# Performance work log

Hardware: AMD Instinct MI355X
Metric: run time of the kernel (lower is better)

## Reference

```python
import jax, jax.numpy as jnp
import numpy as np

B, T, D, H = 2, 2048, 1024, 16
HD = D // H  # head_dim = 64

def setup_inputs() -> dict:
    key = jax.random.key(0)
    ks = jax.random.split(key, 5)
    s = 0.02
    return {
        "x": jax.random.normal(ks[0], (B, T, D), dtype=jnp.float32),
        "w_qkv": jax.random.normal(ks[1], (3 * D, D), dtype=jnp.float32) * s,
        "b_qkv": jax.random.normal(ks[2], (3 * D,), dtype=jnp.float32) * s,
        "w_proj": jax.random.normal(ks[3], (D, D), dtype=jnp.float32) * s,
        "b_proj": jax.random.normal(ks[4], (D,), dtype=jnp.float32) * s,
    }

def reference(x, w_qkv, b_qkv, w_proj, b_proj):
    b, t, c = x.shape
    h, hd = H, HD
    scale = hd ** -0.5
    # qkv projection (torch Linear: x @ W^T + b)
    qkv = x @ w_qkv.T + b_qkv                      # [b, t, 3c]
    q, k, v = jnp.split(qkv, 3, axis=-1)
    # b t (h d) -> b h t d
    reshape = lambda z: z.reshape(b, t, h, hd).transpose(0, 2, 1, 3)
    q, k, v = reshape(q), reshape(k), reshape(v)
    scores = jnp.einsum("bhqd,bhkd->bhqk", q, k) * scale  # [b, h, t, t]
    causal = jnp.triu(jnp.ones((t, t), dtype=bool), k=1)   # True above diag
    scores = jnp.where(causal[None, None], -jnp.inf, scores)
    attn = jax.nn.softmax(scores, axis=-1)
    out = jnp.einsum("bhqk,bhkd->bhqd", attn, v)            # [b, h, t, d]
    out = out.transpose(0, 2, 1, 3).reshape(b, t, c)        # b h t d -> b t (h d)
    return out @ w_proj.T + b_proj
```

## Files before the change

kernel.cpp:

```cpp
#include <hip/hip_runtime.h>
#include <hip/hip_bf16.h>

#define Bq 2
#define Tq 2048
#define Dq 1024
#define Hq 16
#define HDq 64

typedef __attribute__((ext_vector_type(8))) short short8;
typedef __attribute__((ext_vector_type(4))) float f32x4;

__device__ __forceinline__ unsigned short f2bf(float f) {
  union { float f; unsigned int i; } v; v.f = f;
  unsigned int r = v.i + 0x7fffu + ((v.i >> 16) & 1u);
  return (unsigned short)(r >> 16);
}

__device__ __forceinline__ short8 cvt8(const float* __restrict__ g) {
  const float4* gp = (const float4*)g;
  float4 x0 = gp[0], x1 = gp[1];
  short8 v;
  v[0] = (short)f2bf(x0.x); v[1] = (short)f2bf(x0.y);
  v[2] = (short)f2bf(x0.z); v[3] = (short)f2bf(x0.w);
  v[4] = (short)f2bf(x1.x); v[5] = (short)f2bf(x1.y);
  v[6] = (short)f2bf(x1.z); v[7] = (short)f2bf(x1.w);
  return v;
}

__device__ __forceinline__ void async_cp16(const void* g, void* l) {
  __builtin_amdgcn_global_load_lds(
      (const __attribute__((address_space(1))) void*)g,
      (__attribute__((address_space(3))) void*)l, 16, 0, 0);
}

__device__ __forceinline__ void permswap(unsigned &a, unsigned &b) {
  asm("v_permlane32_swap_b32 %0, %1" : "+v"(a), "+v"(b));
  asm("v_permlane16_swap_b32 %0, %1" : "+v"(a), "+v"(b));
}

constexpr int NXC = (Bq * Tq * Dq) / 8;
constexpr int NW1C = (3 * Dq * Dq) / 8;
constexpr int NW2C = (Dq * Dq) / 8;

#define QSCL 0.18033688011112042f

__global__ __launch_bounds__(256)
void cvt_all(const float* __restrict__ x, const float* __restrict__ w1,
             const float* __restrict__ w2, unsigned short* __restrict__ xo,
             unsigned short* __restrict__ w1o, unsigned short* __restrict__ w2o)
{
  int i = blockIdx.x * 256 + threadIdx.x;
  const float* src; unsigned short* dst; int j;
  if (i < NXC)              { src = x;  dst = xo;  j = i; }
  else if (i < NXC + NW1C)  { src = w1; dst = w1o; j = i - NXC; }
  else                      { src = w2; dst = w2o; j = i - NXC - NW1C; }
  *(short8*)&dst[(size_t)j * 8] = cvt8(src + (size_t)j * 8);
}

template<int EPI, int BM_, int BN_>
__global__ __launch_bounds__(256)
void gemm_bt(const unsigned short* __restrict__ Ab, const unsigned short* __restrict__ Wb,
             const float* __restrict__ bias, float* __restrict__ outp,
             int K, int N,
             unsigned short* __restrict__ qo, unsigned short* __restrict__ ko,
             unsigned short* __restrict__ vo)
{
  constexpr int WM = BM_ / 2, WN = BN_ / 2;
  constexpr int NI = WM / 16;
  constexpr int NJ = WN / 16;
  constexpr int NAI = BM_ / 32;
  constexpr int NBI = BN_ / 32;
  __shared__ unsigned short As[2 * BM_ * 32];
  __shared__ unsigned short Bs[2 * BN_ * 32];

  const int t = threadIdx.x;
  const int lane = t & 63, w = t >> 6;
  const int m0 = blockIdx.y * BM_, n0 = blockIdx.x * BN_;
  const int fr = lane & 15, qd = lane >> 4;
  const int wm = (w >> 1) * WM, wn = (w & 1) * WN;

  f32x4 acc[NI][NJ] = {};

  for (int k0 = 0; k0 < K; k0 += 64) {
    __syncthreads();
    #pragma unroll
    for (int j = 0; j < NAI; j++) {
      int G = j * 256 + t;
      int panel = G / (BM_ * 4), rowg = (G / 4) % BM_, colg = G & 3;
      async_cp16(Ab + (size_t)(m0 + rowg) * K + k0 + panel * 32 + colg * 8, &As[G * 8]);
    }
    #pragma unroll
    for (int j = 0; j < NBI; j++) {
      int G = j * 256 + t;
      int panel = G / (BN_ * 4), rowg = (G / 4) % BN_, colg = G & 3;
      async_cp16(Wb + (size_t)(n0 + rowg) * K + k0 + panel * 32 + colg * 8, &Bs[G * 8]);
    }
    __syncthreads();
    #pragma unroll
    for (int kh = 0; kh < 2; kh++) {
      short8 af[NI], bf[NJ];
      #pragma unroll
      for (int ib = 0; ib < NI; ib++)
        af[ib] = *(const short8*)&As[kh * (BM_ * 32) + (wm + ib * 16 + fr) * 32 + qd * 8];
      #pragma unroll
      for (int jb = 0; jb < NJ; jb++)
        bf[jb] = *(const short8*)&Bs[kh * (BN_ * 32) + (wn + jb * 16 + fr) * 32 + qd * 8];
      #pragma unroll
      for (int ib = 0; ib < NI; ib++)
        #pragma unroll
        for (int jb = 0; jb < NJ; jb++)
          acc[ib][jb] = __builtin_amdgcn_mfma_f32_16x16x32_bf16(af[ib], bf[jb], acc[ib][jb], 0, 0, 0);
    }
  }

  #pragma unroll
  for (int jb = 0; jb < NJ; jb++) {
    int col = n0 + wn + jb * 16 + fr;
    float bv = bias[col];
    if (EPI == 0) {
      int which = col >> 10;
      int rem = col & 1023;
      int hh = rem >> 6, dd = rem & 63;
      #pragma unroll
      for (int ib = 0; ib < NI; ib++) {
        int row4 = m0 + wm + ib * 16 + qd * 4;
        int bb = row4 >> 11, tt = row4 & (Tq - 1);
        if (which == 2) {
          unsigned lo = (unsigned)f2bf(acc[ib][jb][0] + bv)
                      | ((unsigned)f2bf(acc[ib][jb][1] + bv) << 16);
          unsigned hi = (unsigned)f2bf(acc[ib][jb][2] + bv)
                      | ((unsigned)f2bf(acc[ib][jb][3] + bv) << 16);
          uint2 pk; pk.x = lo; pk.y = hi;
          *(uint2*)&vo[((size_t)(bb * Hq + hh) * HDq + dd) * Tq + tt] = pk;
        } else {
          unsigned short* dst = (which == 0) ? qo : ko;
          float scl = (which == 0) ? QSCL : 1.0f;
          #pragma unroll
          for (int r = 0; r < 4; r++)
            dst[((size_t)(bb * Hq + hh) * Tq + tt + r) * HDq + dd] =
                f2bf((acc[ib][jb][r] + bv) * scl);
        }
      }
    } else {
      #pragma unroll
      for (int ib = 0; ib < NI; ib++)
        #pragma unroll
        for (int r = 0; r < 4; r++) {
          int row = m0 + wm + ib * 16 + qd * 4 + r;
          outp[(size_t)row * N + col] = acc[ib][jb][r] + bv;
        }
    }
  }
}


template<bool DIAG>
__device__ __forceinline__ void strip_iter(
    const unsigned short* __restrict__ Ksb, const unsigned short* __restrict__ Vtsb,
    const short8 (&aq)[2], const short8 ones,
    int fr, int qd, int off0, int off1, int thr,
    f32x4 (&oacc)[4], f32x4& lacc)
{
  short8 bk[4][2];
  #pragma unroll
  for (int nb = 0; nb < 4; nb++) {
    bk[nb][0] = *(const short8*)&Ksb[(nb * 16 + fr) * 64 + off0];
    bk[nb][1] = *(const short8*)&Ksb[(nb * 16 + fr) * 64 + off1];
  }
  f32x4 s4[4] = {};
  __builtin_amdgcn_s_setprio(1);
  #pragma unroll
  for (int nb = 0; nb < 4; nb++)
    s4[nb] = __builtin_amdgcn_mfma_f32_16x16x32_bf16(bk[nb][0], aq[0], s4[nb], 0, 0, 0);
  #pragma unroll
  for (int nb = 0; nb < 4; nb++)
    s4[nb] = __builtin_amdgcn_mfma_f32_16x16x32_bf16(bk[nb][1], aq[1], s4[nb], 0, 0, 0);
  __builtin_amdgcn_s_setprio(0);

  unsigned x[4][2];
  #pragma unroll
  for (int nb = 0; nb < 4; nb++) {
    float p[4];
    #pragma unroll
    for (int reg = 0; reg < 4; reg++) {
      p[reg] = exp2f(s4[nb][reg]);
      if (DIAG && (nb * 16 + qd * 4 + reg) > thr) p[reg] = 0.f;
    }
    asm("v_cvt_pk_bf16_f32 %0, %1, %2" : "=v"(x[nb][0]) : "v"(p[0]), "v"(p[1]));
    asm("v_cvt_pk_bf16_f32 %0, %1, %2" : "=v"(x[nb][1]) : "v"(p[2]), "v"(p[3]));
  }
  permswap(x[0][0], x[1][0]);
  permswap(x[0][1], x[1][1]);
  permswap(x[2][0], x[3][0]);
  permswap(x[2][1], x[3][1]);

  short8 ap0, ap1;
  {
    union { unsigned u[4]; short8 s; } c0, c1;
    c0.u[0] = x[0][0]; c0.u[1] = x[0][1]; c0.u[2] = x[1][0]; c0.u[3] = x[1][1];
    c1.u[0] = x[2][0]; c1.u[1] = x[2][1]; c1.u[2] = x[3][0]; c1.u[3] = x[3][1];
    ap0 = c0.s; ap1 = c1.s;
  }

  short8 bv[4][2];
  #pragma unroll
  for (int db = 0; db < 4; db++) {
    bv[db][0] = *(const short8*)&Vtsb[(db * 16 + fr) * 64 + off0];
    bv[db][1] = *(const short8*)&Vtsb[(db * 16 + fr) * 64 + off1];
  }
  __builtin_amdgcn_s_setprio(1);
  lacc = __builtin_amdgcn_mfma_f32_16x16x32_bf16(ap0, ones, lacc, 0, 0, 0);
  lacc = __builtin_amdgcn_mfma_f32_16x16x32_bf16(ap1, ones, lacc, 0, 0, 0);
  #pragma unroll
  for (int db = 0; db < 4; db++) {
    oacc[db] = __builtin_amdgcn_mfma_f32_16x16x32_bf16(ap0, bv[db][0], oacc[db], 0, 0, 0);
    oacc[db] = __builtin_amdgcn_mfma_f32_16x16x32_bf16(ap1, bv[db][1], oacc[db], 0, 0, 0);
  }
  __builtin_amdgcn_s_setprio(0);
}

__global__ __launch_bounds__(256, 4)
void attn_fwd(const unsigned short* __restrict__ qb, const unsigned short* __restrict__ kb,
              const unsigned short* __restrict__ vtb, unsigned short* __restrict__ ab)
{
  __shared__ unsigned short Ks[2][64 * 64];
  __shared__ unsigned short Vts[2][64 * 64];

  const int t = threadIdx.x, w = t >> 6, lane = t & 63;
  const int fr = lane & 15, qd = lane >> 4;
  const int bh = blockIdx.x;
  const int s = 31 - (int)blockIdx.y;
  const int s0 = s * 64;
  const int thr = w * 16 + fr;

  short8 aq[2];
  const unsigned short* Qg = qb + ((size_t)bh * Tq + s0) * HDq;
  #pragma unroll
  for (int c = 0; c < 2; c++)
    aq[c] = *(const short8*)(Qg + (w * 16 + fr) * 64 + c * 32 + qd * 8);

  const unsigned short* Kbh = kb + (size_t)bh * Tq * HDq;
  const unsigned short* Vbh = vtb + (size_t)bh * HDq * Tq;

  const int off0 = ((qd ^ (fr & 7)) * 8);
  const int off1 = off0 ^ 32;

  const int G0 = 2 * w * 64 + lane, G1 = G0 + 64;
  const int r0 = G0 >> 3, g0 = (G0 & 7) ^ (r0 & 7);
  const int r1 = G1 >> 3, g1 = (G1 & 7) ^ (r1 & 7);

  short8 ones;
  #pragma unroll
  for (int j = 0; j < 8; j++) ones[j] = (short)0x3F80;

  f32x4 oacc[4] = {};
  f32x4 lacc = {};

  async_cp16(Kbh + (size_t)r0 * 64 + g0 * 8, &Ks[0][G0 * 8]);
  async_cp16(Vbh + (size_t)r0 * Tq + g0 * 8, &Vts[0][G0 * 8]);
  async_cp16(Kbh + (size_t)r1 * 64 + g1 * 8, &Ks[0][G1 * 8]);
  async_cp16(Vbh + (size_t)r1 * Tq + g1 * 8, &Vts[0][G1 * 8]);

  for (int kt = 0; kt < s; kt++) {
    const int cur = kt & 1, nxt = cur ^ 1;
    __syncthreads();
    const size_t kofs = (size_t)(kt + 1) * 64;
    async_cp16(Kbh + (kofs + r0) * 64 + g0 * 8, &Ks[nxt][G0 * 8]);
    async_cp16(Vbh + (size_t)r0 * Tq + kofs + g0 * 8, &Vts[nxt][G0 * 8]);
    async_cp16(Kbh + (kofs + r1) * 64 + g1 * 8, &Ks[nxt][G1 * 8]);
    async_cp16(Vbh + (size_t)r1 * Tq + kofs + g1 * 8, &Vts[nxt][G1 * 8]);
    strip_iter<false>(Ks[cur], Vts[cur], aq, ones, fr, qd, off0, off1, thr, oacc, lacc);
  }
  __syncthreads();
  strip_iter<true>(Ks[s & 1], Vts[s & 1], aq, ones, fr, qd, off0, off1, thr, oacc, lacc);

  #pragma unroll
  for (int reg = 0; reg < 4; reg++) {
    float linv = 1.0f / lacc[reg];
    size_t rowoff = ((size_t)(bh >> 4) * Tq + s0 + w * 16 + qd * 4 + reg) * Dq
                  + (bh & 15) * HDq;
    #pragma unroll
    for (int db = 0; db < 4; db++)
      ab[rowoff + db * 16 + fr] = f2bf(oacc[db][reg] * linv);
  }
}

extern "C" void kernel_launch(void* const* d_in, const int* in_sizes, int n_in,
                              void* d_out, int out_size, void* d_ws, size_t ws_size,
                              hipStream_t stream) {
  const float* x      = (const float*)d_in[0];
  const float* w_qkv  = (const float*)d_in[1];
  const float* b_qkv  = (const float*)d_in[2];
  const float* w_proj = (const float*)d_in[3];
  const float* b_proj = (const float*)d_in[4];
  float* out = (float*)d_out;

  unsigned short* ws = (unsigned short*)d_ws;
  const size_t NE = (size_t)Bq * Hq * Tq * HDq;
  unsigned short* qb  = ws;
  unsigned short* kb  = ws + NE;
  unsigned short* vtb = ws + 2 * NE;
  unsigned short* ab  = ws + 3 * NE;
  unsigned short* xb  = ws + 4 * NE;
  unsigned short* wqb = xb + (size_t)NXC * 8;
  unsigned short* wpb = wqb + (size_t)NW1C * 8;

  dim3 blk(256);
  cvt_all<<<dim3((NXC + NW1C + NW2C) >> 8), blk, 0, stream>>>(x, w_qkv, w_proj, xb, wqb, wpb);

  dim3 g1(3 * Dq / 128, Bq * Tq / 128);
  gemm_bt<0, 128, 128><<<g1, blk, 0, stream>>>(xb, wqb, b_qkv, nullptr,
                                               Dq, 3 * Dq, qb, kb, vtb);
  dim3 g2(Bq * Hq, Tq / 64);
  attn_fwd<<<g2, blk, 0, stream>>>(qb, kb, vtb, ab);
  dim3 g3(Dq / 128, Bq * Tq / 64);
  gemm_bt<1, 64, 128><<<g3, blk, 0, stream>>>(ab, wpb, b_proj, out,
                                              Dq, Dq, nullptr, nullptr, nullptr);
}
```

Baseline: 175.0 us.

## Add 256x256 eight-wave QKV GEMM with phased async staging and MFMA priority

Replaces the 128x128 QKV projection GEMM with a dedicated 256x256-tile kernel using 512 threads (8 waves), a 64-wide K step, XOR-swizzled LDS, and a double buffer whose next-tile loads are split into four phases interleaved with MFMA blocks under raised scheduling priority. The aim is more data reuse per tile and better overlap of global loads with matrix math in the largest GEMM. The trade-off is only 12x16=192 blocks (fewer than CUs per wave of launch on MI355X), heavy register and LDS use (128 KB shared), and many barriers per K step.

```diff
diff --git a/kernel.cpp b/kernel.cpp
--- a/kernel.cpp
+++ b/kernel.cpp
@@ -55,6 +55,145 @@
   else if (i < NXC + NW1C)  { src = w1; dst = w1o; j = i - NXC; }
   else                      { src = w2; dst = w2o; j = i - NXC - NW1C; }
   *(short8*)&dst[(size_t)j * 8] = cvt8(src + (size_t)j * 8);
+}
+
+
+__global__ __launch_bounds__(512, 2)
+void gemm_qkv_8p(const unsigned short* __restrict__ Ab,
+                 const unsigned short* __restrict__ Wb,
+                 const float* __restrict__ bias, int K,
+                 unsigned short* __restrict__ qo, unsigned short* __restrict__ ko,
+                 unsigned short* __restrict__ vo)
+{
+  __shared__ unsigned short As[2][256 * 64];
+  __shared__ unsigned short Bs[2][256 * 64];
+
+  const int t = threadIdx.x;
+  const int lane = t & 63, w = t >> 6;
+  const int fr = lane & 15, qd = lane >> 4;
+  const int wmi = w >> 2, wni = w & 3;
+  const int m0 = blockIdx.y * 256, n0 = blockIdx.x * 256;
+  const int arow_base = wmi * 128;
+  const int brow_base = wni * 64;
+
+  const int Gr0 = t >> 3;
+  const int Gr1 = 64 + Gr0;
+  const int Gc  = (t & 7) ^ (Gr0 & 7);
+
+#define STAGE_HALF(kt1, hh, bufi) do {                                         \
+    const unsigned short* _sb = ((hh) < 2) ? Ab + (size_t)m0 * K               \
+                                           : Wb + (size_t)n0 * K;              \
+    unsigned short* _lb = ((hh) < 2) ? &As[bufi][0] : &Bs[bufi][0];            \
+    const int _h = (hh) & 1;                                                   \
+    async_cp16(_sb + (size_t)(_h * 128 + Gr0) * K + (kt1) * 64 + Gc * 8,       \
+               _lb + _h * 8192 + t * 8);                                       \
+    async_cp16(_sb + (size_t)(_h * 128 + Gr1) * K + (kt1) * 64 + Gc * 8,       \
+               _lb + _h * 8192 + 4096 + t * 8);                                \
+  } while (0)
+
+#define READ_AF(rg) do {                                                       \
+    _Pragma("unroll")                                                          \
+    for (int ibs = 0; ibs < 4; ibs++) {                                        \
+      const int r = arow_base + (rg) * 64 + ibs * 16 + fr;                     \
+      af[ibs][0] = *(const short8*)&As[c][r * 64 + ((qd ^ (r & 7)) * 8)];      \
+      af[ibs][1] = *(const short8*)&As[c][r * 64 + (((4 + qd) ^ (r & 7)) * 8)];\
+    } } while (0)
+
+#define READ_BF(cg) do {                                                       \
+    _Pragma("unroll")                                                          \
+    for (int jbs = 0; jbs < 2; jbs++) {                                        \
+      const int r = brow_base + (cg) * 32 + jbs * 16 + fr;                     \
+      bf[jbs][0] = *(const short8*)&Bs[c][r * 64 + ((qd ^ (r & 7)) * 8)];      \
+      bf[jbs][1] = *(const short8*)&Bs[c][r * 64 + (((4 + qd) ^ (r & 7)) * 8)];\
+    } } while (0)
+
+#define MM16(rg, cg) do {                                                      \
+    __builtin_amdgcn_s_setprio(1);                                             \
+    _Pragma("unroll")                                                          \
+    for (int ibs = 0; ibs < 4; ibs++)                                          \
+      _Pragma("unroll")                                                        \
+      for (int jbs = 0; jbs < 2; jbs++) {                                      \
+        acc[(rg)*4+ibs][(cg)*2+jbs] = __builtin_amdgcn_mfma_f32_16x16x32_bf16( \
+            af[ibs][0], bf[jbs][0], acc[(rg)*4+ibs][(cg)*2+jbs], 0, 0, 0);     \
+        acc[(rg)*4+ibs][(cg)*2+jbs] = __builtin_amdgcn_mfma_f32_16x16x32_bf16( \
+            af[ibs][1], bf[jbs][1], acc[(rg)*4+ibs][(cg)*2+jbs], 0, 0, 0);     \
+      }                                                                        \
+    __builtin_amdgcn_s_setprio(0); } while (0)
+
+#define BAR() do { asm volatile("" ::: "memory");                              \
+    __builtin_amdgcn_s_barrier(); asm volatile("" ::: "memory"); } while (0)
+
+  f32x4 acc[8][4] = {};
+  short8 af[4][2], bf[2][2];
+
+  STAGE_HALF(0, 0, 0); STAGE_HALF(0, 1, 0);
+  STAGE_HALF(0, 2, 0); STAGE_HALF(0, 3, 0);
+
+  const int KT = K >> 6;
+  for (int kt = 0; kt < KT; kt++) {
+    const int c = kt & 1;
+    const bool pf = (kt + 1 < KT);
+    if (pf) {
+      STAGE_HALF(kt + 1, 0, c ^ 1);
+      asm volatile("s_waitcnt vmcnt(2)" ::: "memory");
+    } else {
+      asm volatile("s_waitcnt vmcnt(0)" ::: "memory");
+    }
+    __builtin_amdgcn_s_barrier();
+    READ_AF(0); READ_BF(0);
+    BAR();
+    MM16(0, 0);
+    BAR();
+    READ_BF(1);
+    if (pf) STAGE_HALF(kt + 1, 1, c ^ 1);
+    BAR();
+    MM16(0, 1);
+    BAR();
+    READ_AF(1);
+    if (pf) STAGE_HALF(kt + 1, 2, c ^ 1);
+    BAR();
+    MM16(1, 1);
+    BAR();
+    READ_BF(0);
+    if (pf) STAGE_HALF(kt + 1, 3, c ^ 1);
+    BAR();
+    MM16(1, 0);
+    BAR();
+  }
+
+  #pragma unroll
+  for (int jb = 0; jb < 4; jb++) {
+    int col = n0 + wni * 64 + jb * 16 + fr;
+    float bv = bias[col];
+    int which = col >> 10;
+    int rem = col & 1023;
+    int hh = rem >> 6, dd = rem & 63;
+    #pragma unroll
+    for (int ib = 0; ib < 8; ib++) {
+      int row4 = m0 + wmi * 128 + ib * 16 + qd * 4;
+      int bb = row4 >> 11, tt = row4 & (Tq - 1);
+      if (which == 2) {
+        unsigned lo = (unsigned)f2bf(acc[ib][jb][0] + bv)
+                    | ((unsigned)f2bf(acc[ib][jb][1] + bv) << 16);
+        unsigned hi = (unsigned)f2bf(acc[ib][jb][2] + bv)
+                    | ((unsigned)f2bf(acc[ib][jb][3] + bv) << 16);
+        uint2 pk; pk.x = lo; pk.y = hi;
+        *(uint2*)&vo[((size_t)(bb * Hq + hh) * HDq + dd) * Tq + tt] = pk;
+      } else {
+        unsigned short* dst = (which == 0) ? qo : ko;
+        float scl = (which == 0) ? QSCL : 1.0f;
+        #pragma unroll
+        for (int r = 0; r < 4; r++)
+          dst[((size_t)(bb * Hq + hh) * Tq + tt + r) * HDq + dd] =
+              f2bf((acc[ib][jb][r] + bv) * scl);
+      }
+    }
+  }
+#undef STAGE_HALF
+#undef READ_AF
+#undef READ_BF
+#undef MM16
+#undef BAR
 }
 
 template<int EPI, int BM_, int BN_>
@@ -308,11 +447,12 @@
   dim3 blk(256);
   cvt_all<<<dim3((NXC + NW1C + NW2C) >> 8), blk, 0, stream>>>(x, w_qkv, w_proj, xb, wqb, wpb);
 
-  dim3 g1(3 * Dq / 128, Bq * Tq / 128);
-  gemm_bt<0, 128, 128><<<g1, blk, 0, stream>>>(xb, wqb, b_qkv, nullptr,
-                                               Dq, 3 * Dq, qb, kb, vtb);
+  dim3 g1(3 * Dq / 256, Bq * Tq / 256);
+  gemm_qkv_8p<<<g1, dim3(512), 0, stream>>>(xb, wqb, b_qkv, Dq, qb, kb, vtb);
+
   dim3 g2(Bq * Hq, Tq / 64);
   attn_fwd<<<g2, blk, 0, stream>>>(qb, kb, vtb, ab);
+
   dim3 g3(Dq / 128, Bq * Tq / 64);
   gemm_bt<1, 64, 128><<<g3, blk, 0, stream>>>(ab, wpb, b_proj, out,
                                               Dq, Dq, nullptr, nullptr, nullptr);
```

After: 180.5 us. 1.03x slower.

## Pair short and long causal query strips per block to balance attention work

Applied to the files above, without the earlier changes.

Each attention block now handles two query strips, p and 31-p. They share the same K/V tiles loaded into shared memory, so every block gets equal work under the causal mask and K/V reuse doubles for the overlapping prefix. The grid halves to 16 x 32 blocks and launch bounds drop to 2 blocks per CU to make room for the doubled accumulators and Q fragments. The cost is higher register pressure, lower occupancy and fewer blocks in flight.

```diff
diff --git a/kernel.cpp b/kernel.cpp
--- a/kernel.cpp
+++ b/kernel.cpp
@@ -155,7 +155,7 @@
 
 
 template<bool DIAG>
-__device__ __forceinline__ void strip_iter(
+__device__ __forceinline__ void strip_one(
     const unsigned short* __restrict__ Ksb, const unsigned short* __restrict__ Vtsb,
     const short8 (&aq)[2], const short8 ones,
     int fr, int qd, int off0, int off1, int thr,
@@ -219,7 +219,88 @@
   __builtin_amdgcn_s_setprio(0);
 }
 
-__global__ __launch_bounds__(256, 4)
+template<bool SMALLDIAG>
+__device__ __forceinline__ void strip_dual(
+    const unsigned short* __restrict__ Ksb, const unsigned short* __restrict__ Vtsb,
+    const short8 (&aqB)[2], const short8 (&aqA)[2], const short8 ones,
+    int fr, int qd, int off0, int off1, int thr,
+    f32x4 (&oB)[4], f32x4& lB, f32x4 (&oA)[4], f32x4& lA)
+{
+  short8 bk[4][2];
+  #pragma unroll
+  for (int nb = 0; nb < 4; nb++) {
+    bk[nb][0] = *(const short8*)&Ksb[(nb * 16 + fr) * 64 + off0];
+    bk[nb][1] = *(const short8*)&Ksb[(nb * 16 + fr) * 64 + off1];
+  }
+  f32x4 sB[4] = {}, sA[4] = {};
+  __builtin_amdgcn_s_setprio(1);
+  #pragma unroll
+  for (int nb = 0; nb < 4; nb++) {
+    sB[nb] = __builtin_amdgcn_mfma_f32_16x16x32_bf16(bk[nb][0], aqB[0], sB[nb], 0, 0, 0);
+    sA[nb] = __builtin_amdgcn_mfma_f32_16x16x32_bf16(bk[nb][0], aqA[0], sA[nb], 0, 0, 0);
+  }
+  #pragma unroll
+  for (int nb = 0; nb < 4; nb++) {
+    sB[nb] = __builtin_amdgcn_mfma_f32_16x16x32_bf16(bk[nb][1], aqB[1], sB[nb], 0, 0, 0);
+    sA[nb] = __builtin_amdgcn_mfma_f32_16x16x32_bf16(bk[nb][1], aqA[1], sA[nb], 0, 0, 0);
+  }
+  __builtin_amdgcn_s_setprio(0);
+
+  unsigned xB[4][2], xA[4][2];
+  #pragma unroll
+  for (int nb = 0; nb < 4; nb++) {
+    float pB[4], pA[4];
+    #pragma unroll
+    for (int reg = 0; reg < 4; reg++) {
+      pB[reg] = exp2f(sB[nb][reg]);
+      pA[reg] = exp2f(sA[nb][reg]);
+      if (SMALLDIAG && (nb * 16 + qd * 4 + reg) > thr) pA[reg] = 0.f;
+    }
+    asm("v_cvt_pk_bf16_f32 %0, %1, %2" : "=v"(xB[nb][0]) : "v"(pB[0]), "v"(pB[1]));
+    asm("v_cvt_pk_bf16_f32 %0, %1, %2" : "=v"(xB[nb][1]) : "v"(pB[2]), "v"(pB[3]));
+    asm("v_cvt_pk_bf16_f32 %0, %1, %2" : "=v"(xA[nb][0]) : "v"(pA[0]), "v"(pA[1]));
+    asm("v_cvt_pk_bf16_f32 %0, %1, %2" : "=v"(xA[nb][1]) : "v"(pA[2]), "v"(pA[3]));
+  }
+  permswap(xB[0][0], xB[1][0]); permswap(xB[0][1], xB[1][1]);
+  permswap(xB[2][0], xB[3][0]); permswap(xB[2][1], xB[3][1]);
+  permswap(xA[0][0], xA[1][0]); permswap(xA[0][1], xA[1][1]);
+  permswap(xA[2][0], xA[3][0]); permswap(xA[2][1], xA[3][1]);
+
+  short8 apB0, apB1, apA0, apA1;
+  {
+    union { unsigned u[4]; short8 s; } c0, c1, c2, c3;
+    c0.u[0] = xB[0][0]; c0.u[1] = xB[0][1]; c0.u[2] = xB[1][0]; c0.u[3] = xB[1][1];
+    c1.u[0] = xB[2][0]; c1.u[1] = xB[2][1]; c1.u[2] = xB[3][0]; c1.u[3] = xB[3][1];
+    c2.u[0] = xA[0][0]; c2.u[1] = xA[0][1]; c2.u[2] = xA[1][0]; c2.u[3] = xA[1][1];
+    c3.u[0] = xA[2][0]; c3.u[1] = xA[2][1]; c3.u[2] = xA[3][0]; c3.u[3] = xA[3][1];
+    apB0 = c0.s; apB1 = c1.s; apA0 = c2.s; apA1 = c3.s;
+  }
+
+  short8 bv[4][2];
+  #pragma unroll
+  for (int db = 0; db < 4; db++) {
+    bv[db][0] = *(const short8*)&Vtsb[(db * 16 + fr) * 64 + off0];
+    bv[db][1] = *(const short8*)&Vtsb[(db * 16 + fr) * 64 + off1];
+  }
+  __builtin_amdgcn_s_setprio(1);
+  lB = __builtin_amdgcn_mfma_f32_16x16x32_bf16(apB0, ones, lB, 0, 0, 0);
+  lA = __builtin_amdgcn_mfma_f32_16x16x32_bf16(apA0, ones, lA, 0, 0, 0);
+  lB = __builtin_amdgcn_mfma_f32_16x16x32_bf16(apB1, ones, lB, 0, 0, 0);
+  lA = __builtin_amdgcn_mfma_f32_16x16x32_bf16(apA1, ones, lA, 0, 0, 0);
+  #pragma unroll
+  for (int db = 0; db < 4; db++) {
+    oB[db] = __builtin_amdgcn_mfma_f32_16x16x32_bf16(apB0, bv[db][0], oB[db], 0, 0, 0);
+    oA[db] = __builtin_amdgcn_mfma_f32_16x16x32_bf16(apA0, bv[db][0], oA[db], 0, 0, 0);
+  }
+  #pragma unroll
+  for (int db = 0; db < 4; db++) {
+    oB[db] = __builtin_amdgcn_mfma_f32_16x16x32_bf16(apB1, bv[db][1], oB[db], 0, 0, 0);
+    oA[db] = __builtin_amdgcn_mfma_f32_16x16x32_bf16(apA1, bv[db][1], oA[db], 0, 0, 0);
+  }
+  __builtin_amdgcn_s_setprio(0);
+}
+
+__global__ __launch_bounds__(256, 2)
 void attn_fwd(const unsigned short* __restrict__ qb, const unsigned short* __restrict__ kb,
               const unsigned short* __restrict__ vtb, unsigned short* __restrict__ ab)
 {
@@ -228,16 +309,22 @@
 
   const int t = threadIdx.x, w = t >> 6, lane = t & 63;
   const int fr = lane & 15, qd = lane >> 4;
-  const int bh = blockIdx.x;
-  const int s = 31 - (int)blockIdx.y;
-  const int s0 = s * 64;
+  const int p = blockIdx.x;
+  const int bh = blockIdx.y;
+  const int sB = 31 - p, sA = p;
+  const int s0t[2] = { sB * 64, sA * 64 };
   const int thr = w * 16 + fr;
 
-  short8 aq[2];
-  const unsigned short* Qg = qb + ((size_t)bh * Tq + s0) * HDq;
-  #pragma unroll
-  for (int c = 0; c < 2; c++)
-    aq[c] = *(const short8*)(Qg + (w * 16 + fr) * 64 + c * 32 + qd * 8);
+  short8 aqB[2], aqA[2];
+  {
+    const unsigned short* QgB = qb + ((size_t)bh * Tq + s0t[0]) * HDq;
+    const unsigned short* QgA = qb + ((size_t)bh * Tq + s0t[1]) * HDq;
+    #pragma unroll
+    for (int c = 0; c < 2; c++) {
+      aqB[c] = *(const short8*)(QgB + (w * 16 + fr) * 64 + c * 32 + qd * 8);
+      aqA[c] = *(const short8*)(QgA + (w * 16 + fr) * 64 + c * 32 + qd * 8);
+    }
+  }
 
   const unsigned short* Kbh = kb + (size_t)bh * Tq * HDq;
   const unsigned short* Vbh = vtb + (size_t)bh * HDq * Tq;
@@ -253,35 +340,53 @@
   #pragma unroll
   for (int j = 0; j < 8; j++) ones[j] = (short)0x3F80;
 
-  f32x4 oacc[4] = {};
-  f32x4 lacc = {};
+  f32x4 oB[4] = {}, oA[4] = {};
+  f32x4 lB = {}, lA = {};
 
   async_cp16(Kbh + (size_t)r0 * 64 + g0 * 8, &Ks[0][G0 * 8]);
   async_cp16(Vbh + (size_t)r0 * Tq + g0 * 8, &Vts[0][G0 * 8]);
   async_cp16(Kbh + (size_t)r1 * 64 + g1 * 8, &Ks[0][G1 * 8]);
   async_cp16(Vbh + (size_t)r1 * Tq + g1 * 8, &Vts[0][G1 * 8]);
 
-  for (int kt = 0; kt < s; kt++) {
-    const int cur = kt & 1, nxt = cur ^ 1;
+  for (int kt = 0; kt <= sB; kt++) {
+    const int cur = kt & 1;
     __syncthreads();
-    const size_t kofs = (size_t)(kt + 1) * 64;
-    async_cp16(Kbh + (kofs + r0) * 64 + g0 * 8, &Ks[nxt][G0 * 8]);
-    async_cp16(Vbh + (size_t)r0 * Tq + kofs + g0 * 8, &Vts[nxt][G0 * 8]);
-    async_cp16(Kbh + (kofs + r1) * 64 + g1 * 8, &Ks[nxt][G1 * 8]);
-    async_cp16(Vbh + (size_t)r1 * Tq + kofs + g1 * 8, &Vts[nxt][G1 * 8]);
-    strip_iter<false>(Ks[cur], Vts[cur], aq, ones, fr, qd, off0, off1, thr, oacc, lacc);
-  }
-  __syncthreads();
-  strip_iter<true>(Ks[s & 1], Vts[s & 1], aq, ones, fr, qd, off0, off1, thr, oacc, lacc);
+    if (kt < sB) {
+      const int nxt = cur ^ 1;
+      const size_t kofs = (size_t)(kt + 1) * 64;
+      async_cp16(Kbh + (kofs + r0) * 64 + g0 * 8, &Ks[nxt][G0 * 8]);
+      async_cp16(Vbh + (size_t)r0 * Tq + kofs + g0 * 8, &Vts[nxt][G0 * 8]);
+      async_cp16(Kbh + (kofs + r1) * 64 + g1 * 8, &Ks[nxt][G1 * 8]);
+      async_cp16(Vbh + (size_t)r1 * Tq + kofs + g1 * 8, &Vts[nxt][G1 * 8]);
+    }
+    if (kt < sA) {
+      strip_dual<false>(Ks[cur], Vts[cur], aqB, aqA, ones,
+                        fr, qd, off0, off1, thr, oB, lB, oA, lA);
+    } else if (kt == sA) {
+      strip_dual<true >(Ks[cur], Vts[cur], aqB, aqA, ones,
+                        fr, qd, off0, off1, thr, oB, lB, oA, lA);
+    } else if (kt == sB) {
+      strip_one<true >(Ks[cur], Vts[cur], aqB, ones,
+                       fr, qd, off0, off1, thr, oB, lB);
+    } else {
+      strip_one<false>(Ks[cur], Vts[cur], aqB, ones,
+                       fr, qd, off0, off1, thr, oB, lB);
+    }
+  }
 
   #pragma unroll
   for (int reg = 0; reg < 4; reg++) {
-    float linv = 1.0f / lacc[reg];
-    size_t rowoff = ((size_t)(bh >> 4) * Tq + s0 + w * 16 + qd * 4 + reg) * Dq
-                  + (bh & 15) * HDq;
-    #pragma unroll
-    for (int db = 0; db < 4; db++)
-      ab[rowoff + db * 16 + fr] = f2bf(oacc[db][reg] * linv);
+    float linvB = 1.0f / lB[reg];
+    float linvA = 1.0f / lA[reg];
+    size_t rowB = ((size_t)(bh >> 4) * Tq + s0t[0] + w * 16 + qd * 4 + reg) * Dq
+                + (bh & 15) * HDq;
+    size_t rowA = ((size_t)(bh >> 4) * Tq + s0t[1] + w * 16 + qd * 4 + reg) * Dq
+                + (bh & 15) * HDq;
+    #pragma unroll
+    for (int db = 0; db < 4; db++) {
+      ab[rowB + db * 16 + fr] = f2bf(oB[db][reg] * linvB);
+      ab[rowA + db * 16 + fr] = f2bf(oA[db][reg] * linvA);
+    }
   }
 }
 
@@ -311,8 +416,10 @@
   dim3 g1(3 * Dq / 128, Bq * Tq / 128);
   gemm_bt<0, 128, 128><<<g1, blk, 0, stream>>>(xb, wqb, b_qkv, nullptr,
                                                Dq, 3 * Dq, qb, kb, vtb);
-  dim3 g2(Bq * Hq, Tq / 64);
+
+  dim3 g2(16, Bq * Hq);
   attn_fwd<<<g2, blk, 0, stream>>>(qb, kb, vtb, ab);
+
   dim3 g3(Dq / 128, Bq * Tq / 64);
   gemm_bt<1, 64, 128><<<g3, blk, 0, stream>>>(ab, wpb, b_proj, out,
                                               Dq, Dq, nullptr, nullptr, nullptr);
```

After: 184.7 us. +5.5%, slower.
